# Kernel tuning notes

Measured on AMD Instinct MI355X. Metric: run time of the kernel, lower is better.

The kernel has to match this reference:

```python
import jax, jax.numpy as jnp
import numpy as np

EMBED_DIM = 1024
NUM_HEADS = 16
HEAD_DIM = EMBED_DIM // NUM_HEADS


def setup_inputs() -> dict:
    key = jax.random.key(0)
    ks = jax.random.split(key, 5)
    B, N, E = 2, 2048, EMBED_DIM
    scale = E ** -0.5
    return {
        "x": jax.random.normal(ks[0], (B, N, E), dtype=jnp.float32),
        "w_qkv": jax.random.normal(ks[1], (E, 3 * E), dtype=jnp.float32) * scale,
        "b_qkv": jnp.zeros((3 * E,), dtype=jnp.float32),
        "w_proj": jax.random.normal(ks[2], (E, E), dtype=jnp.float32) * scale,
        "b_proj": jnp.zeros((E,), dtype=jnp.float32),
    }


def reference(x, w_qkv, b_qkv, w_proj, b_proj):
    B, N, E = x.shape
    H, D = NUM_HEADS, HEAD_DIM
    qkv = x @ w_qkv + b_qkv                      # [B,N,3E]
    qkv = qkv.reshape(B, N, 3, H, D)
    q = qkv[:, :, 0].transpose(0, 2, 1, 3)        # [B,H,N,D]
    k = qkv[:, :, 1].transpose(0, 2, 1, 3)
    v = qkv[:, :, 2].transpose(0, 2, 1, 3)
    attn = jnp.einsum('bhnd,bhmd->bhnm', q, k) * (D ** -0.5)
    attn = jax.nn.softmax(attn, axis=-1)          # dropout is identity in eval mode
    out = jnp.einsum('bhnm,bhmd->bhnd', attn, v)  # [B,H,N,D]
    out = out.transpose(0, 2, 1, 3).reshape(B, N, E)
    return out @ w_proj + b_proj
```

## Files before the change

kernel.cpp:

```cpp
#include <hip/hip_runtime.h>
#include <hip/hip_bf16.h>
#include <cstdint>
#include <cstddef>


typedef __attribute__((ext_vector_type(8))) short short8;
typedef __attribute__((ext_vector_type(4))) short short4v;
typedef __attribute__((ext_vector_type(4))) float f32x4;

#define MFMA16(a, b, c) __builtin_amdgcn_mfma_f32_16x16x32_bf16((a), (b), (c), 0, 0, 0)
#define EXP2F(x) __builtin_amdgcn_exp2f(x)

__device__ __forceinline__ float b2f(short s) {
  union { unsigned u; float f; } x; x.u = ((unsigned)(unsigned short)s) << 16; return x.f;
}
__device__ __forceinline__ short f2b(float f) {
  union { float f; unsigned u; } x; x.f = f;
  unsigned r = x.u + 0x7fffu + ((x.u >> 16) & 1u);
  return (short)(r >> 16);
}
__device__ __forceinline__ void async_lds16(const void* g, void* l) {
  __builtin_amdgcn_global_load_lds(
      (const __attribute__((address_space(1))) void*)g,
      (__attribute__((address_space(3))) void*)l, 16, 0, 0);
}

__global__ __launch_bounds__(256) void cast_f32_bf16(const float* __restrict__ in,
                                                     short* __restrict__ out, int n4) {
  int idx = blockIdx.x * 256 + threadIdx.x;
  if (idx < n4) {
    f32x4 v = ((const f32x4*)in)[idx];
    short4v o;
    #pragma unroll
    for (int e = 0; e < 4; ++e) o[e] = f2b(v[e]);
    ((short4v*)out)[idx] = o;
  }
}

__global__ __launch_bounds__(256) void transpose_cast(const float* __restrict__ in,
                                                      short* __restrict__ out,
                                                      int R, int C) {
  __shared__ float tile[32][33];
  int c0 = blockIdx.x * 32, r0 = blockIdx.y * 32;
  int tx = threadIdx.x, ty = threadIdx.y;
  #pragma unroll
  for (int i = ty; i < 32; i += 8)
    tile[i][tx] = in[(size_t)(r0 + i) * C + c0 + tx];
  __syncthreads();
  #pragma unroll
  for (int i = ty; i < 32; i += 8)
    out[(size_t)(c0 + i) * R + r0 + tx] = f2b(tile[tx][i]);
}

__global__ __launch_bounds__(256) void gemm_qkv(const short* __restrict__ xb,
                                                const short* __restrict__ wT,
                                                const float* __restrict__ bias,
                                                short* __restrict__ Qb,
                                                short* __restrict__ Kb,
                                                short* __restrict__ Vt) {
  __shared__ short lds_a[128 * 32];
  __shared__ short lds_b[128 * 32];
  const int tid = threadIdx.x, wid = tid >> 6, lane = tid & 63;
  const int lg = lane >> 4, lr = lane & 15;
  const int lin = blockIdx.x;
  const int swz = (lin & 7) * 96 + (lin >> 3);
  const int m0 = (swz & 31) * 128, n0 = (swz >> 5) * 128;
  const int wr = wid >> 1, wc = wid & 1;
  const int K = 1024;

  f32x4 acc[4][4];
  #pragma unroll
  for (int i = 0; i < 4; ++i)
    #pragma unroll
    for (int j = 0; j < 4; ++j) acc[i][j] = (f32x4)0.0f;

  for (int k0 = 0; k0 < K; k0 += 32) {
    #pragma unroll
    for (int it = 0; it < 2; ++it) {
      int chunk = it * 256 + tid;
      int row = chunk >> 2, kc = (chunk & 3) * 8;
      async_lds16(xb + (size_t)(m0 + row) * K + k0 + kc, lds_a + chunk * 8);
      async_lds16(wT + (size_t)(n0 + row) * K + k0 + kc, lds_b + chunk * 8);
    }
    __syncthreads();
    short8 af[4], bfr[4];
    #pragma unroll
    for (int i = 0; i < 4; ++i)
      af[i] = *(const short8*)&lds_a[(wr * 64 + i * 16 + lr) * 32 + lg * 8];
    #pragma unroll
    for (int j = 0; j < 4; ++j)
      bfr[j] = *(const short8*)&lds_b[(wc * 64 + j * 16 + lr) * 32 + lg * 8];
    #pragma unroll
    for (int i = 0; i < 4; ++i)
      #pragma unroll
      for (int j = 0; j < 4; ++j) acc[i][j] = MFMA16(af[i], bfr[j], acc[i][j]);
    __syncthreads();
  }

  #pragma unroll
  for (int i = 0; i < 4; ++i) {
    int gm = m0 + wr * 64 + i * 16 + lg * 4;
    int bb = gm >> 11, n = gm & 2047;
    #pragma unroll
    for (int j = 0; j < 4; ++j) {
      int gc = n0 + wc * 64 + j * 16 + lr;
      float bv = bias[gc];
      int which = gc >> 10;
      int h = (gc >> 6) & 15;
      int dd = gc & 63;
      size_t qkbase = ((size_t)((bb * 16 + h) * 2048 + n)) * 64 + dd;
      if (which == 2) {
        size_t vtbase = ((size_t)((bb * 16 + h) * 64 + dd)) * 2048 + n;
        short4v pv;
        #pragma unroll
        for (int r = 0; r < 4; ++r) pv[r] = f2b(acc[i][j][r] + bv);
        *(short4v*)&Vt[vtbase] = pv;
      } else {
        short* dst = (which == 0) ? Qb : Kb;
        #pragma unroll
        for (int r = 0; r < 4; ++r)
          dst[qkbase + (size_t)r * 64] = f2b(acc[i][j][r] + bv);
      }
    }
  }
}

__global__ __launch_bounds__(512) void attn_fwd(const short* __restrict__ Qb,
                                                const short* __restrict__ Kb,
                                                const short* __restrict__ Vt,
                                                short* __restrict__ aob) {
  __shared__ short k_lds[2][64 * 64];
  __shared__ short v_lds[2][64 * 64];
  __shared__ short p_lds[8 * 16 * 64];
  const int tid = threadIdx.x, wid = tid >> 6, lane = tid & 63;
  const int lg = lane >> 4, lr = lane & 15;
  const int lin = blockIdx.x;
  const int swz = (lin & 7) * 64 + (lin >> 3);
  const int qt = swz & 15, bh = swz >> 4;
  const int q0 = qt * 128 + wid * 16;
  const short* Qbh = Qb + (size_t)bh * 2048 * 64;
  const short* Kbh = Kb + (size_t)bh * 2048 * 64;
  const short* Vbh = Vt + (size_t)bh * 64 * 2048;
  const int rm = (lr >> 1) & 7;

  const int srow = tid >> 3;
  const int ssrc = ((tid & 7) ^ ((srow >> 1) & 7)) * 8;

  short8 qf[2];
  #pragma unroll
  for (int kk = 0; kk < 2; ++kk) {
    qf[kk] = *(const short8*)(Qbh + (size_t)(q0 + lr) * 64 + kk * 32 + lg * 8);
    #pragma unroll
    for (int e = 0; e < 8; ++e) qf[kk][e] = f2b(b2f(qf[kk][e]) * 0.1803368801f);
  }

  f32x4 o[4];
  #pragma unroll
  for (int dt = 0; dt < 4; ++dt) o[dt] = (f32x4)0.0f;
  float m_ = -__builtin_inff(), l_ = 0.0f;

  async_lds16(Kbh + (size_t)srow * 64 + ssrc, &k_lds[0][tid * 8]);
  async_lds16(Vbh + (size_t)srow * 2048 + 0 + ssrc, &v_lds[0][tid * 8]);
  asm volatile("s_waitcnt vmcnt(0)" ::: "memory");
  __syncthreads();

  for (int t = 0; t < 32; ++t) {
    const int cur = t & 1;
    if (t + 1 < 32) {
      int kvn = (t + 1) * 64;
      async_lds16(Kbh + (size_t)(kvn + srow) * 64 + ssrc, &k_lds[cur ^ 1][tid * 8]);
      async_lds16(Vbh + (size_t)srow * 2048 + kvn + ssrc, &v_lds[cur ^ 1][tid * 8]);
    }

    f32x4 s[4];
    #pragma unroll
    for (int jt = 0; jt < 4; ++jt) s[jt] = (f32x4)0.0f;
    #pragma unroll
    for (int jt = 0; jt < 4; ++jt)
      #pragma unroll
      for (int kk = 0; kk < 2; ++kk) {
        short8 kf = *(const short8*)&k_lds[cur][(jt * 16 + lr) * 64 +
                                               (((kk * 4 + lg) ^ rm) * 8)];
        s[jt] = MFMA16(kf, qf[kk], s[jt]);
      }

    float pmax = s[0][0];
    #pragma unroll
    for (int jt = 0; jt < 4; ++jt)
      #pragma unroll
      for (int r = 0; r < 4; ++r) pmax = fmaxf(pmax, s[jt][r]);
    pmax = fmaxf(pmax, __shfl_xor(pmax, 16));
    pmax = fmaxf(pmax, __shfl_xor(pmax, 32));
    if (!__all(pmax - m_ <= 8.0f)) {
      float mn = fmaxf(m_, pmax);
      float corr = EXP2F(m_ - mn);
      m_ = mn;
      l_ *= corr;
      #pragma unroll
      for (int dt = 0; dt < 4; ++dt)
        #pragma unroll
        for (int r = 0; r < 4; ++r) o[dt][r] *= corr;
    }
    float ps = 0.0f;
    #pragma unroll
    for (int jt = 0; jt < 4; ++jt)
      #pragma unroll
      for (int r = 0; r < 4; ++r) {
        float p = EXP2F(s[jt][r] - m_);
        s[jt][r] = p;
        ps += p;
      }
    ps += __shfl_xor(ps, 16);
    ps += __shfl_xor(ps, 32);
    l_ += ps;

    #pragma unroll
    for (int jt = 0; jt < 4; ++jt) {
      short4v pv;
      #pragma unroll
      for (int r = 0; r < 4; ++r) pv[r] = f2b(s[jt][r]);
      *(short4v*)&p_lds[wid * 1024 + lr * 64 +
                        (((jt * 2 + (lg >> 1)) ^ rm) * 8) + (lg & 1) * 4] = pv;
    }
    asm volatile("s_waitcnt lgkmcnt(0)" ::: "memory");
    __builtin_amdgcn_sched_barrier(0);

    #pragma unroll
    for (int kk = 0; kk < 2; ++kk) {
      short8 pa = *(const short8*)&p_lds[wid * 1024 + lr * 64 +
                                         (((kk * 4 + lg) ^ rm) * 8)];
      #pragma unroll
      for (int dt = 0; dt < 4; ++dt) {
        short8 vb = *(const short8*)&v_lds[cur][(dt * 16 + lr) * 64 +
                                               (((kk * 4 + lg) ^ rm) * 8)];
        o[dt] = MFMA16(vb, pa, o[dt]);
      }
    }
    asm volatile("s_waitcnt vmcnt(0)" ::: "memory");
    __syncthreads();
  }

  const int bb = bh >> 4, h = bh & 15;
  const float inv_l = __frcp_rn(l_);
  #pragma unroll
  for (int dt = 0; dt < 4; ++dt) {
    short4v ov;
    #pragma unroll
    for (int r = 0; r < 4; ++r) ov[r] = f2b(o[dt][r] * inv_l);
    *(short4v*)&aob[(size_t)(bb * 2048 + q0 + lr) * 1024 + h * 64 + dt * 16 + lg * 4] = ov;
  }
}

__global__ __launch_bounds__(256) void gemm_proj(const short* __restrict__ aob,
                                                 const short* __restrict__ wT,
                                                 const float* __restrict__ bias,
                                                 float* __restrict__ out) {
  __shared__ short lds_a[64 * 32];
  __shared__ short lds_b[128 * 32];
  const int tid = threadIdx.x, wid = tid >> 6, lane = tid & 63;
  const int lg = lane >> 4, lr = lane & 15;
  const int lin = blockIdx.x;
  const int swz = (lin & 7) * 64 + (lin >> 3);
  const int m0 = (swz & 63) * 64, n0 = (swz >> 6) * 128;
  const int mw = wid >> 1, nw = wid & 1;
  const int K = 1024;

  f32x4 acc[2][4];
  #pragma unroll
  for (int i = 0; i < 2; ++i)
    #pragma unroll
    for (int j = 0; j < 4; ++j) acc[i][j] = (f32x4)0.0f;

  for (int k0 = 0; k0 < K; k0 += 32) {
    {
      int row = tid >> 2, kc = (tid & 3) * 8;
      async_lds16(aob + (size_t)(m0 + row) * K + k0 + kc, lds_a + tid * 8);
    }
    #pragma unroll
    for (int it = 0; it < 2; ++it) {
      int chunk = it * 256 + tid;
      int row = chunk >> 2, kc = (chunk & 3) * 8;
      async_lds16(wT + (size_t)(n0 + row) * K + k0 + kc, lds_b + chunk * 8);
    }
    __syncthreads();
    short8 af[2], bfr[4];
    #pragma unroll
    for (int i = 0; i < 2; ++i)
      af[i] = *(const short8*)&lds_a[(mw * 32 + i * 16 + lr) * 32 + lg * 8];
    #pragma unroll
    for (int j = 0; j < 4; ++j)
      bfr[j] = *(const short8*)&lds_b[(nw * 64 + j * 16 + lr) * 32 + lg * 8];
    #pragma unroll
    for (int i = 0; i < 2; ++i)
      #pragma unroll
      for (int j = 0; j < 4; ++j) acc[i][j] = MFMA16(af[i], bfr[j], acc[i][j]);
    __syncthreads();
  }

  #pragma unroll
  for (int i = 0; i < 2; ++i) {
    int gm = m0 + mw * 32 + i * 16 + lg * 4;
    #pragma unroll
    for (int j = 0; j < 4; ++j) {
      int gc = n0 + nw * 64 + j * 16 + lr;
      float bv = bias[gc];
      #pragma unroll
      for (int r = 0; r < 4; ++r)
        out[(size_t)(gm + r) * 1024 + gc] = acc[i][j][r] + bv;
    }
  }
}

extern "C" void kernel_launch(void* const* d_in, const int* in_sizes, int n_in,
                              void* d_out, int out_size, void* d_ws, size_t ws_size,
                              hipStream_t stream) {
  const float* x     = (const float*)d_in[0];
  const float* wqkv  = (const float*)d_in[1];
  const float* bqkv  = (const float*)d_in[2];
  const float* wproj = (const float*)d_in[3];
  const float* bproj = (const float*)d_in[4];
  float* out = (float*)d_out;

  char* ws = (char*)d_ws;
  short* xb     = (short*)ws; ws += (size_t)4096 * 1024 * 2;
  short* wqkvT  = (short*)ws; ws += (size_t)3072 * 1024 * 2;
  short* wprojT = (short*)ws; ws += (size_t)1024 * 1024 * 2;
  short* Qb     = (short*)ws; ws += (size_t)32 * 2048 * 64 * 2;
  short* Kb     = (short*)ws; ws += (size_t)32 * 2048 * 64 * 2;
  short* Vt     = (short*)ws; ws += (size_t)32 * 64 * 2048 * 2;
  short* aob    = (short*)ws; ws += (size_t)4096 * 1024 * 2;

  cast_f32_bf16<<<4096, 256, 0, stream>>>(x, xb, 4096 * 1024 / 4);
  transpose_cast<<<dim3(96, 32), dim3(32, 8), 0, stream>>>(wqkv, wqkvT, 1024, 3072);
  transpose_cast<<<dim3(32, 32), dim3(32, 8), 0, stream>>>(wproj, wprojT, 1024, 1024);
  gemm_qkv<<<768, 256, 0, stream>>>(xb, wqkvT, bqkv, Qb, Kb, Vt);
  attn_fwd<<<512, 512, 0, stream>>>(Qb, Kb, Vt, aob);
  gemm_proj<<<512, 256, 0, stream>>>(aob, wprojT, bproj, out);
}
```

Baseline: 214.5 us.

## Double GEMM K-step to 64 with XOR-swizzled LDS and prioritise attention MFMAs

```diff
diff --git a/kernel.cpp b/kernel.cpp
--- a/kernel.cpp
+++ b/kernel.cpp
@@ -52,14 +52,14 @@
     out[(size_t)(c0 + i) * R + r0 + tx] = f2b(tile[tx][i]);
 }
 
-__global__ __launch_bounds__(256) void gemm_qkv(const short* __restrict__ xb,
-                                                const short* __restrict__ wT,
-                                                const float* __restrict__ bias,
-                                                short* __restrict__ Qb,
-                                                short* __restrict__ Kb,
-                                                short* __restrict__ Vt) {
-  __shared__ short lds_a[128 * 32];
-  __shared__ short lds_b[128 * 32];
+__global__ __launch_bounds__(256, 3) void gemm_qkv(const short* __restrict__ xb,
+                                                   const short* __restrict__ wT,
+                                                   const float* __restrict__ bias,
+                                                   short* __restrict__ Qb,
+                                                   short* __restrict__ Kb,
+                                                   short* __restrict__ Vt) {
+  __shared__ short lds_a[128 * 64];
+  __shared__ short lds_b[128 * 64];
   const int tid = threadIdx.x, wid = tid >> 6, lane = tid & 63;
   const int lg = lane >> 4, lr = lane & 15;
   const int lin = blockIdx.x;
@@ -67,6 +67,7 @@
   const int m0 = (swz & 31) * 128, n0 = (swz >> 5) * 128;
   const int wr = wid >> 1, wc = wid & 1;
   const int K = 1024;
+  const int sm = lr & 7;
 
   f32x4 acc[4][4];
   #pragma unroll
@@ -74,26 +75,31 @@
     #pragma unroll
     for (int j = 0; j < 4; ++j) acc[i][j] = (f32x4)0.0f;
 
-  for (int k0 = 0; k0 < K; k0 += 32) {
-    #pragma unroll
-    for (int it = 0; it < 2; ++it) {
+  for (int k0 = 0; k0 < K; k0 += 64) {
+    #pragma unroll
+    for (int it = 0; it < 4; ++it) {
       int chunk = it * 256 + tid;
-      int row = chunk >> 2, kc = (chunk & 3) * 8;
+      int row = chunk >> 3, kc = ((chunk & 7) ^ (row & 7)) * 8;
       async_lds16(xb + (size_t)(m0 + row) * K + k0 + kc, lds_a + chunk * 8);
       async_lds16(wT + (size_t)(n0 + row) * K + k0 + kc, lds_b + chunk * 8);
     }
     __syncthreads();
-    short8 af[4], bfr[4];
-    #pragma unroll
-    for (int i = 0; i < 4; ++i)
-      af[i] = *(const short8*)&lds_a[(wr * 64 + i * 16 + lr) * 32 + lg * 8];
-    #pragma unroll
-    for (int j = 0; j < 4; ++j)
-      bfr[j] = *(const short8*)&lds_b[(wc * 64 + j * 16 + lr) * 32 + lg * 8];
-    #pragma unroll
-    for (int i = 0; i < 4; ++i)
-      #pragma unroll
-      for (int j = 0; j < 4; ++j) acc[i][j] = MFMA16(af[i], bfr[j], acc[i][j]);
+    #pragma unroll
+    for (int kk = 0; kk < 2; ++kk) {
+      short8 af[4], bfr[4];
+      #pragma unroll
+      for (int i = 0; i < 4; ++i)
+        af[i] = *(const short8*)&lds_a[(wr * 64 + i * 16 + lr) * 64 +
+                                       (((kk * 4 + lg) ^ sm) * 8)];
+      #pragma unroll
+      for (int j = 0; j < 4; ++j)
+        bfr[j] = *(const short8*)&lds_b[(wc * 64 + j * 16 + lr) * 64 +
+                                        (((kk * 4 + lg) ^ sm) * 8)];
+      #pragma unroll
+      for (int i = 0; i < 4; ++i)
+        #pragma unroll
+        for (int j = 0; j < 4; ++j) acc[i][j] = MFMA16(af[i], bfr[j], acc[i][j]);
+    }
     __syncthreads();
   }
 
@@ -175,6 +181,7 @@
     f32x4 s[4];
     #pragma unroll
     for (int jt = 0; jt < 4; ++jt) s[jt] = (f32x4)0.0f;
+    __builtin_amdgcn_s_setprio(1);
     #pragma unroll
     for (int jt = 0; jt < 4; ++jt)
       #pragma unroll
@@ -183,6 +190,7 @@
                                                (((kk * 4 + lg) ^ rm) * 8)];
         s[jt] = MFMA16(kf, qf[kk], s[jt]);
       }
+    __builtin_amdgcn_s_setprio(0);
 
     float pmax = s[0][0];
     #pragma unroll
@@ -225,6 +233,7 @@
     asm volatile("s_waitcnt lgkmcnt(0)" ::: "memory");
     __builtin_amdgcn_sched_barrier(0);
 
+    __builtin_amdgcn_s_setprio(1);
     #pragma unroll
     for (int kk = 0; kk < 2; ++kk) {
       short8 pa = *(const short8*)&p_lds[wid * 1024 + lr * 64 +
@@ -236,6 +245,7 @@
         o[dt] = MFMA16(vb, pa, o[dt]);
       }
     }
+    __builtin_amdgcn_s_setprio(0);
     asm volatile("s_waitcnt vmcnt(0)" ::: "memory");
     __syncthreads();
   }
@@ -251,12 +261,12 @@
   }
 }
 
-__global__ __launch_bounds__(256) void gemm_proj(const short* __restrict__ aob,
-                                                 const short* __restrict__ wT,
-                                                 const float* __restrict__ bias,
-                                                 float* __restrict__ out) {
-  __shared__ short lds_a[64 * 32];
-  __shared__ short lds_b[128 * 32];
+__global__ __launch_bounds__(256, 2) void gemm_proj(const short* __restrict__ aob,
+                                                    const short* __restrict__ wT,
+                                                    const float* __restrict__ bias,
+                                                    float* __restrict__ out) {
+  __shared__ short lds_a[64 * 64];
+  __shared__ short lds_b[128 * 64];
   const int tid = threadIdx.x, wid = tid >> 6, lane = tid & 63;
   const int lg = lane >> 4, lr = lane & 15;
   const int lin = blockIdx.x;
@@ -264,6 +274,7 @@
   const int m0 = (swz & 63) * 64, n0 = (swz >> 6) * 128;
   const int mw = wid >> 1, nw = wid & 1;
   const int K = 1024;
+  const int sm = lr & 7;
 
   f32x4 acc[2][4];
   #pragma unroll
@@ -271,29 +282,36 @@
     #pragma unroll
     for (int j = 0; j < 4; ++j) acc[i][j] = (f32x4)0.0f;
 
-  for (int k0 = 0; k0 < K; k0 += 32) {
-    {
-      int row = tid >> 2, kc = (tid & 3) * 8;
-      async_lds16(aob + (size_t)(m0 + row) * K + k0 + kc, lds_a + tid * 8);
-    }
+  for (int k0 = 0; k0 < K; k0 += 64) {
     #pragma unroll
     for (int it = 0; it < 2; ++it) {
       int chunk = it * 256 + tid;
-      int row = chunk >> 2, kc = (chunk & 3) * 8;
+      int row = chunk >> 3, kc = ((chunk & 7) ^ (row & 7)) * 8;
+      async_lds16(aob + (size_t)(m0 + row) * K + k0 + kc, lds_a + chunk * 8);
+    }
+    #pragma unroll
+    for (int it = 0; it < 4; ++it) {
+      int chunk = it * 256 + tid;
+      int row = chunk >> 3, kc = ((chunk & 7) ^ (row & 7)) * 8;
       async_lds16(wT + (size_t)(n0 + row) * K + k0 + kc, lds_b + chunk * 8);
     }
     __syncthreads();
-    short8 af[2], bfr[4];
-    #pragma unroll
-    for (int i = 0; i < 2; ++i)
-      af[i] = *(const short8*)&lds_a[(mw * 32 + i * 16 + lr) * 32 + lg * 8];
-    #pragma unroll
-    for (int j = 0; j < 4; ++j)
-      bfr[j] = *(const short8*)&lds_b[(nw * 64 + j * 16 + lr) * 32 + lg * 8];
-    #pragma unroll
-    for (int i = 0; i < 2; ++i)
-      #pragma unroll
-      for (int j = 0; j < 4; ++j) acc[i][j] = MFMA16(af[i], bfr[j], acc[i][j]);
+    #pragma unroll
+    for (int kk = 0; kk < 2; ++kk) {
+      short8 af[2], bfr[4];
+      #pragma unroll
+      for (int i = 0; i < 2; ++i)
+        af[i] = *(const short8*)&lds_a[(mw * 32 + i * 16 + lr) * 64 +
+                                       (((kk * 4 + lg) ^ sm) * 8)];
+      #pragma unroll
+      for (int j = 0; j < 4; ++j)
+        bfr[j] = *(const short8*)&lds_b[(nw * 64 + j * 16 + lr) * 64 +
+                                        (((kk * 4 + lg) ^ sm) * 8)];
+      #pragma unroll
+      for (int i = 0; i < 2; ++i)
+        #pragma unroll
+        for (int j = 0; j < 4; ++j) acc[i][j] = MFMA16(af[i], bfr[j], acc[i][j]);
+    }
     __syncthreads();
   }
 
```

Result: faster. 198.9 us (-7.3%).
